# Performance work log

Measured on AMD Instinct MI355X. Metric: run time of the kernel, lower is better.

Reference implementation:

```python
import jax, jax.numpy as jnp
import numpy as np

T, LDIMS, HID, HID2 = 768, 256, 512, 512


def setup_inputs() -> dict:
    key = jax.random.key(0)
    ks = jax.random.split(key, 8)
    s = 0.05  # small init scale keeps tanh out of saturation
    return {
        "x": jax.random.normal(ks[0], (T, 2, LDIMS), dtype=jnp.float32),
        "hidLayerFOH": jax.random.normal(ks[1], (2 * LDIMS, HID), dtype=jnp.float32) * s,
        "hidLayerFOM": jax.random.normal(ks[2], (2 * LDIMS, HID), dtype=jnp.float32) * s,
        "catBias": jax.random.normal(ks[3], (2 * HID,), dtype=jnp.float32) * s,
        "hid2Layer": jax.random.normal(ks[4], (2 * HID, HID2), dtype=jnp.float32) * s,
        "hid2Bias": jax.random.normal(ks[5], (HID2,), dtype=jnp.float32) * s,
        "outLayer": jax.random.normal(ks[6], (HID2, 1), dtype=jnp.float32) * s,
        "outBias": jax.random.normal(ks[7], (1,), dtype=jnp.float32) * s,
    }


def reference(x, hidLayerFOH, hidLayerFOM, catBias, hid2Layer, hid2Bias, outLayer, outBias):
    # x: [T, 2, ldims] -> concat forward/backward LSTM states -> [T, 2*ldims]
    xc = x.reshape(x.shape[0], -1)
    Hf = xc @ hidLayerFOH  # [T, HID] headfov per token
    Mf = xc @ hidLayerFOM  # [T, HID] modfov per token
    # Original: tanh(concat([headfov_i, modfov_j]) + catBias) @ hid2Layer.
    # tanh is elementwise, so split the concat: act halves separately, then
    # split hid2Layer into top/bottom blocks — same math, no [T,T,2H] tensor.
    actH = jnp.tanh(Hf + catBias[:HID])   # [T, HID]
    actM = jnp.tanh(Mf + catBias[HID:])   # [T, HID]
    AH = actH @ hid2Layer[:HID]           # [T, HID2]
    AM = actM @ hid2Layer[HID:]           # [T, HID2]
    # Pairwise second layer: Z[i,j] = tanh(AH[i] + AM[j] + hid2Bias)
    Z = jnp.tanh(AH[:, None, :] + AM[None, :, :] + hid2Bias)  # [T, T, HID2]
    scores = jnp.einsum("ijh,h->ij", Z, outLayer[:, 0]) + outBias[0]  # [T, T]
    return scores
```

## Files before the change

### kernel.cpp

```cpp
#include <hip/hip_runtime.h>

#define TT 768
#define KD 512
#define NC 1024
#define RLN2_2 2.8853900817779268f

typedef short short8 __attribute__((ext_vector_type(8)));
typedef float f32x4  __attribute__((ext_vector_type(4)));
typedef float f32x2  __attribute__((ext_vector_type(2)));

__device__ __forceinline__ float fast_exp2(float x) {
#if __has_builtin(__builtin_amdgcn_exp2f)
    return __builtin_amdgcn_exp2f(x);
#else
    return exp2f(x);
#endif
}
__device__ __forceinline__ float fast_rcp(float x) {
#if __has_builtin(__builtin_amdgcn_rcpf)
    return __builtin_amdgcn_rcpf(x);
#else
    return 1.0f / x;
#endif
}
__device__ __forceinline__ float fast_tanh(float x) {
    float e = fast_exp2(x * RLN2_2);
    return fmaf(-2.0f, fast_rcp(e + 1.0f), 1.0f);
}
__device__ __forceinline__ ushort f2bf(float f) {
    uint u = __float_as_uint(f);
    u += 0x7fff + ((u >> 16) & 1);
    return (ushort)(u >> 16);
}

__global__ __launch_bounds__(256) void k_prep(
    const float* __restrict__ x, const float* __restrict__ foh,
    const float* __restrict__ fom, const float* __restrict__ hid2,
    ushort* __restrict__ xb, ushort* __restrict__ b1t, ushort* __restrict__ h2t)
{
    const int b = blockIdx.x, t = threadIdx.x;
    if (b < 96) {
        int base = b * 4096 + t * 16;
        #pragma unroll
        for (int q = 0; q < 4; ++q) {
            float4 v = *(const float4*)&x[base + q * 4];
            ushort4 o; o.x = f2bf(v.x); o.y = f2bf(v.y); o.z = f2bf(v.z); o.w = f2bf(v.w);
            *(ushort4*)&xb[base + q * 4] = o;
        }
        return;
    }
    __shared__ float tile[64][65];
    const float* src; ushort* dst; int R, C, r0, c0;
    if (b < 160)      { int bb = b - 96;  src = foh;  dst = b1t;             R = 512;  C = 512; r0 = (bb >> 3) * 64; c0 = (bb & 7) * 64; }
    else if (b < 224) { int bb = b - 160; src = fom;  dst = b1t + 512 * 512; R = 512;  C = 512; r0 = (bb >> 3) * 64; c0 = (bb & 7) * 64; }
    else              { int bb = b - 224; src = hid2; dst = h2t;             R = 1024; C = 512; r0 = (bb >> 3) * 64; c0 = (bb & 7) * 64; }
    const int ty = t >> 4, tx = t & 15;
    #pragma unroll
    for (int q = 0; q < 4; ++q) {
        float4 v = *(const float4*)&src[(r0 + ty + q * 16) * C + c0 + tx * 4];
        tile[ty + q * 16][tx * 4 + 0] = v.x;
        tile[ty + q * 16][tx * 4 + 1] = v.y;
        tile[ty + q * 16][tx * 4 + 2] = v.z;
        tile[ty + q * 16][tx * 4 + 3] = v.w;
    }
    __syncthreads();
    #pragma unroll
    for (int q = 0; q < 4; ++q) {
        int cl = ty + q * 16;
        ushort4 o;
        o.x = f2bf(tile[tx * 4 + 0][cl]);
        o.y = f2bf(tile[tx * 4 + 1][cl]);
        o.z = f2bf(tile[tx * 4 + 2][cl]);
        o.w = f2bf(tile[tx * 4 + 3][cl]);
        *(ushort4*)&dst[(c0 + cl) * R + r0 + tx * 4] = o;
    }
}

__global__ __launch_bounds__(64) void k_gemm1(
    const ushort* __restrict__ xb, const ushort* __restrict__ b1t,
    const float* __restrict__ catBias, ushort* __restrict__ act)
{
    const int lane = threadIdx.x;
    const int n0 = blockIdx.x * 32;
    const int m0 = blockIdx.y * 32;
    const int lrow = lane & 15, lk = (lane >> 4) * 8;

    const ushort* pa0 = &xb[(m0 + lrow) * KD + lk];
    const ushort* pa1 = pa0 + 16 * KD;
    const ushort* pb0 = &b1t[(n0 + lrow) * KD + lk];
    const ushort* pb1 = pb0 + 16 * KD;

    f32x4 acc[2][2] = {};
    #pragma unroll 4
    for (int k0 = 0; k0 < KD; k0 += 32) {
        short8 a0 = *(const short8*)(pa0 + k0);
        short8 a1 = *(const short8*)(pa1 + k0);
        short8 b0 = *(const short8*)(pb0 + k0);
        short8 b1 = *(const short8*)(pb1 + k0);
        acc[0][0] = __builtin_amdgcn_mfma_f32_16x16x32_bf16(a0, b0, acc[0][0], 0, 0, 0);
        acc[0][1] = __builtin_amdgcn_mfma_f32_16x16x32_bf16(a0, b1, acc[0][1], 0, 0, 0);
        acc[1][0] = __builtin_amdgcn_mfma_f32_16x16x32_bf16(a1, b0, acc[1][0], 0, 0, 0);
        acc[1][1] = __builtin_amdgcn_mfma_f32_16x16x32_bf16(a1, b1, acc[1][1], 0, 0, 0);
    }
    const int crow = (lane >> 4) * 4, ccol = lane & 15;
    #pragma unroll
    for (int nf = 0; nf < 2; ++nf) {
        int col = n0 + nf * 16 + ccol;
        float cb = catBias[col];
        #pragma unroll
        for (int mf = 0; mf < 2; ++mf) {
            #pragma unroll
            for (int r = 0; r < 4; ++r) {
                int row = m0 + mf * 16 + crow + r;
                act[row * NC + col] = f2bf(fast_tanh(acc[mf][nf][r] + cb));
            }
        }
    }
}

__global__ __launch_bounds__(64) void k_gemm2(
    const ushort* __restrict__ act, const ushort* __restrict__ h2t,
    const float* __restrict__ hid2Bias, float* __restrict__ pw)
{
    const int lane = threadIdx.x;
    const int n0 = blockIdx.x * 32;
    const int m0 = blockIdx.y * 32;
    const bool top = (blockIdx.x < 16);
    const int koff = top ? 0 : 512;
    const int nc0  = top ? n0 : n0 - 512;
    const int lrow = lane & 15, lk = (lane >> 4) * 8;

    const ushort* pa0 = &act[(m0 + lrow) * NC + koff + lk];
    const ushort* pa1 = pa0 + 16 * NC;
    const ushort* pb0 = &h2t[(nc0 + lrow) * NC + koff + lk];
    const ushort* pb1 = pb0 + 16 * NC;

    f32x4 acc[2][2] = {};
    #pragma unroll 4
    for (int k0 = 0; k0 < KD; k0 += 32) {
        short8 a0 = *(const short8*)(pa0 + k0);
        short8 a1 = *(const short8*)(pa1 + k0);
        short8 b0 = *(const short8*)(pb0 + k0);
        short8 b1 = *(const short8*)(pb1 + k0);
        acc[0][0] = __builtin_amdgcn_mfma_f32_16x16x32_bf16(a0, b0, acc[0][0], 0, 0, 0);
        acc[0][1] = __builtin_amdgcn_mfma_f32_16x16x32_bf16(a0, b1, acc[0][1], 0, 0, 0);
        acc[1][0] = __builtin_amdgcn_mfma_f32_16x16x32_bf16(a1, b0, acc[1][0], 0, 0, 0);
        acc[1][1] = __builtin_amdgcn_mfma_f32_16x16x32_bf16(a1, b1, acc[1][1], 0, 0, 0);
    }
    const int crow = (lane >> 4) * 4, ccol = lane & 15;
    #pragma unroll
    for (int nf = 0; nf < 2; ++nf) {
        int col = n0 + nf * 16 + ccol;
        float hb = top ? hid2Bias[col] : 0.0f;
        #pragma unroll
        for (int mf = 0; mf < 2; ++mf) {
            #pragma unroll
            for (int r = 0; r < 4; ++r) {
                int row = m0 + mf * 16 + crow + r;
                pw[row * NC + col] = fast_exp2(RLN2_2 * (acc[mf][nf][r] + hb));
            }
        }
    }
}

__global__ __launch_bounds__(256) void k_pair(
    const float* __restrict__ pw, const float* __restrict__ w,
    const float* __restrict__ outBias, float* __restrict__ out)
{
    __shared__ float Ea[4][16][18];
    __shared__ float Em[4][16][18];
    __shared__ float wl[512];

    const int t    = threadIdx.x;
    const int wv   = t >> 6, lane = t & 63;
    const int bid  = blockIdx.x;
    const int sw   = (bid & 7) * 288 + (bid >> 3);
    const int it = sw / 48, jt = sw % 48;
    const int i0 = it * 16, j0 = jt * 16;
    const int hb0 = wv * 128;

    *(float2*)&wl[hb0 + lane * 2] = *(const float2*)&w[hb0 + lane * 2];
    {
        float4 wa = *(const float4*)&w[lane * 8];
        float4 wb = *(const float4*)&w[lane * 8 + 4];
        float ls = (wa.x + wa.y) + (wa.z + wa.w) + (wb.x + wb.y) + (wb.z + wb.w);
        #pragma unroll
        for (int d = 1; d < 64; d <<= 1) ls += __shfl_xor(ls, d, 64);
        wl[0] = wl[0];
        __asm__ volatile("" ::: );
        #define LSUM_READY ls
        {
            const float lsum = LSUM_READY;

            const int sr = lane >> 2;
            const int sc = (lane & 3) * 4;
            const float* srcA = &pw[(i0 + sr) * NC + hb0 + sc];
            const float* srcM = &pw[(j0 + sr) * NC + 512 + hb0 + sc];

            const int li = lane >> 3, lj = lane & 7;

            float4 fa = *(const float4*)(srcA);
            float4 fm = *(const float4*)(srcM);

            const f32x2 one2 = {1.0f, 1.0f};
            f32x2 accA[2] = {}, accB[2] = {};

            #pragma unroll 1
            for (int c = 0; c < 8; ++c) {
                const int hh = c * 16;
                *(float4*)&Ea[wv][sr][sc] = fa;
                *(float4*)&Em[wv][sr][sc] = fm;
                if (c < 7) {
                    fa = *(const float4*)(srcA + hh + 16);
                    fm = *(const float4*)(srcM + hh + 16);
                }
                #pragma unroll
                for (int hq = 0; hq < 4; ++hq) {
                    float4 e0 = *(const float4*)&Ea[wv][2 * li    ][hq * 4];
                    float4 e1 = *(const float4*)&Ea[wv][2 * li + 1][hq * 4];
                    float4 f0 = *(const float4*)&Em[wv][2 * lj    ][hq * 4];
                    float4 f1 = *(const float4*)&Em[wv][2 * lj + 1][hq * 4];
                    float4 w4 = *(const float4*)&wl[hb0 + hh + hq * 4];
                    #define PKQUAD(DA, DB, WH, ACCA, ACCB)                   \
                    {                                                        \
                        f32x2 Q  = DA * DB;                                  \
                        float pr = Q.x * Q.y;                                \
                        float R  = fast_rcp(pr);                             \
                        float RW = R * (WH);                                 \
                        f32x2 T  = (f32x2){Q.y, Q.x} * RW;                   \
                        ACCA = __builtin_elementwise_fma(T, DB, ACCA);       \
                        ACCB = __builtin_elementwise_fma(T, DA, ACCB);       \
                    }
                    #define HSTEP(H, S)                                                     \
                    {                                                                       \
                        f32x2 F  = {f0.H, f1.H};                                            \
                        f32x2 D0 = __builtin_elementwise_fma((f32x2){e0.H, e0.H}, F, one2); \
                        f32x2 D1 = __builtin_elementwise_fma((f32x2){e1.H, e1.H}, F, one2); \
                        PKQUAD(D0, D1, w4.H, accA[S], accB[S])                              \
                    }
                    HSTEP(x, 0) HSTEP(y, 1) HSTEP(z, 0) HSTEP(w, 1)
                    #undef HSTEP
                    #undef PKQUAD
                }
            }

            f32x2 s0 = accA[0] + accA[1];
            f32x2 s1 = accB[0] + accB[1];

            float* partial = (float*)Ea;
            __syncthreads();
            if (wv >= 1) {
                float* p = partial + (wv - 1) * 256 + lane * 4;
                p[0] = s0.x; p[1] = s0.y; p[2] = s1.x; p[3] = s1.y;
            }
            __syncthreads();
            if (wv == 0) {
                const float base = lsum + outBias[0];
                float t00 = s0.x, t01 = s0.y, t10 = s1.x, t11 = s1.y;
                #pragma unroll
                for (int q = 0; q < 3; ++q) {
                    const float* p = partial + q * 256 + lane * 4;
                    t00 += p[0]; t01 += p[1]; t10 += p[2]; t11 += p[3];
                }
                const int gi = i0 + 2 * li, gj = j0 + 2 * lj;
                float2 o0, o1;
                o0.x = fmaf(-2.f, t00, base);
                o0.y = fmaf(-2.f, t01, base);
                o1.x = fmaf(-2.f, t10, base);
                o1.y = fmaf(-2.f, t11, base);
                *(float2*)&out[gi * TT + gj]       = o0;
                *(float2*)&out[(gi + 1) * TT + gj] = o1;
            }
        }
        #undef LSUM_READY
    }
}

extern "C" void kernel_launch(void* const* d_in, const int* in_sizes, int n_in,
                              void* d_out, int out_size, void* d_ws, size_t ws_size,
                              hipStream_t stream) {
    const float* x        = (const float*)d_in[0];
    const float* foh      = (const float*)d_in[1];
    const float* fom      = (const float*)d_in[2];
    const float* catBias  = (const float*)d_in[3];
    const float* hid2     = (const float*)d_in[4];
    const float* hid2Bias = (const float*)d_in[5];
    const float* outLayer = (const float*)d_in[6];
    const float* outBias  = (const float*)d_in[7];
    float* out = (float*)d_out;

    char* wsb = (char*)d_ws;
    float*  pw  = (float*)(wsb);
    ushort* act = (ushort*)(wsb + 3145728);
    ushort* xb  = (ushort*)(wsb + 4718592);
    ushort* b1t = (ushort*)(wsb + 5505024);
    ushort* h2t = (ushort*)(wsb + 6553600);

    k_prep <<<dim3(352),    256, 0, stream>>>(x, foh, fom, hid2, xb, b1t, h2t);
    k_gemm1<<<dim3(32, 24),  64, 0, stream>>>(xb, b1t, catBias, act);
    k_gemm2<<<dim3(32, 24),  64, 0, stream>>>(act, h2t, hid2Bias, pw);
    k_pair <<<dim3(2304),   256, 0, stream>>>(pw, outLayer, outBias, out);
}
```

Before: 61.07 us.

## Split-K across two waves in GEMMs and shrink prep blocks to 64 threads

Both GEMM kernels now run two wavefronts per block, each covering half of K. The partial accumulators are reduced through shared memory before the epilogue, which halves the serial K-loop length per wave and doubles the number of waves in flight. The prep kernel switches to 64-thread blocks with 32x32 transpose tiles, so four times as many blocks are launched. The pair kernel is only restructured syntactically by removing a redundant scope and macro. The changes add an LDS reduction and a barrier per GEMM block.

```diff
diff --git a/kernel.cpp b/kernel.cpp
--- a/kernel.cpp
+++ b/kernel.cpp
@@ -33,14 +33,14 @@
     return (ushort)(u >> 16);
 }
 
-__global__ __launch_bounds__(256) void k_prep(
+__global__ __launch_bounds__(64) void k_prep(
     const float* __restrict__ x, const float* __restrict__ foh,
     const float* __restrict__ fom, const float* __restrict__ hid2,
     ushort* __restrict__ xb, ushort* __restrict__ b1t, ushort* __restrict__ h2t)
 {
-    const int b = blockIdx.x, t = threadIdx.x;
-    if (b < 96) {
-        int base = b * 4096 + t * 16;
+    const int b = blockIdx.x, lane = threadIdx.x;
+    if (b < 384) {
+        int base = b * 1024 + lane * 16;
         #pragma unroll
         for (int q = 0; q < 4; ++q) {
             float4 v = *(const float4*)&x[base + q * 4];
@@ -49,24 +49,26 @@
         }
         return;
     }
-    __shared__ float tile[64][65];
-    const float* src; ushort* dst; int R, C, r0, c0;
-    if (b < 160)      { int bb = b - 96;  src = foh;  dst = b1t;             R = 512;  C = 512; r0 = (bb >> 3) * 64; c0 = (bb & 7) * 64; }
-    else if (b < 224) { int bb = b - 160; src = fom;  dst = b1t + 512 * 512; R = 512;  C = 512; r0 = (bb >> 3) * 64; c0 = (bb & 7) * 64; }
-    else              { int bb = b - 224; src = hid2; dst = h2t;             R = 1024; C = 512; r0 = (bb >> 3) * 64; c0 = (bb & 7) * 64; }
-    const int ty = t >> 4, tx = t & 15;
+    __shared__ float tile[32][33];
+    int bb = b - 384;
+    const float* src; ushort* dst; int R, C;
+    if (bb < 256)      { src = foh;  dst = b1t;             R = 512;  C = 512; }
+    else if (bb < 512) { src = fom;  dst = b1t + 512 * 512; R = 512;  C = 512; bb -= 256; }
+    else               { src = hid2; dst = h2t;             R = 1024; C = 512; bb -= 512; }
+    const int r0 = (bb >> 4) * 32, c0 = (bb & 15) * 32;
+    const int ty = lane >> 3, tx = lane & 7;
     #pragma unroll
     for (int q = 0; q < 4; ++q) {
-        float4 v = *(const float4*)&src[(r0 + ty + q * 16) * C + c0 + tx * 4];
-        tile[ty + q * 16][tx * 4 + 0] = v.x;
-        tile[ty + q * 16][tx * 4 + 1] = v.y;
-        tile[ty + q * 16][tx * 4 + 2] = v.z;
-        tile[ty + q * 16][tx * 4 + 3] = v.w;
+        float4 v = *(const float4*)&src[(r0 + ty + q * 8) * C + c0 + tx * 4];
+        tile[ty + q * 8][tx * 4 + 0] = v.x;
+        tile[ty + q * 8][tx * 4 + 1] = v.y;
+        tile[ty + q * 8][tx * 4 + 2] = v.z;
+        tile[ty + q * 8][tx * 4 + 3] = v.w;
     }
     __syncthreads();
     #pragma unroll
     for (int q = 0; q < 4; ++q) {
-        int cl = ty + q * 16;
+        int cl = ty + q * 8;
         ushort4 o;
         o.x = f2bf(tile[tx * 4 + 0][cl]);
         o.y = f2bf(tile[tx * 4 + 1][cl]);
@@ -76,23 +78,26 @@
     }
 }
 
-__global__ __launch_bounds__(64) void k_gemm1(
+__global__ __launch_bounds__(128) void k_gemm1(
     const ushort* __restrict__ xb, const ushort* __restrict__ b1t,
     const float* __restrict__ catBias, ushort* __restrict__ act)
 {
-    const int lane = threadIdx.x;
+    __shared__ float ps[64][20];
+    const int t = threadIdx.x;
+    const int kv = t >> 6, lane = t & 63;
     const int n0 = blockIdx.x * 32;
     const int m0 = blockIdx.y * 32;
     const int lrow = lane & 15, lk = (lane >> 4) * 8;
-
-    const ushort* pa0 = &xb[(m0 + lrow) * KD + lk];
+    const int kbase = kv * 256;
+
+    const ushort* pa0 = &xb[(m0 + lrow) * KD + kbase + lk];
     const ushort* pa1 = pa0 + 16 * KD;
-    const ushort* pb0 = &b1t[(n0 + lrow) * KD + lk];
+    const ushort* pb0 = &b1t[(n0 + lrow) * KD + kbase + lk];
     const ushort* pb1 = pb0 + 16 * KD;
 
     f32x4 acc[2][2] = {};
     #pragma unroll 4
-    for (int k0 = 0; k0 < KD; k0 += 32) {
+    for (int k0 = 0; k0 < 256; k0 += 32) {
         short8 a0 = *(const short8*)(pa0 + k0);
         short8 a1 = *(const short8*)(pa1 + k0);
         short8 b0 = *(const short8*)(pb0 + k0);
@@ -102,42 +107,58 @@
         acc[1][0] = __builtin_amdgcn_mfma_f32_16x16x32_bf16(a1, b0, acc[1][0], 0, 0, 0);
         acc[1][1] = __builtin_amdgcn_mfma_f32_16x16x32_bf16(a1, b1, acc[1][1], 0, 0, 0);
     }
-    const int crow = (lane >> 4) * 4, ccol = lane & 15;
-    #pragma unroll
-    for (int nf = 0; nf < 2; ++nf) {
-        int col = n0 + nf * 16 + ccol;
-        float cb = catBias[col];
-        #pragma unroll
-        for (int mf = 0; mf < 2; ++mf) {
+    if (kv == 1) {
+        *(f32x4*)&ps[lane][0]  = acc[0][0];
+        *(f32x4*)&ps[lane][4]  = acc[0][1];
+        *(f32x4*)&ps[lane][8]  = acc[1][0];
+        *(f32x4*)&ps[lane][12] = acc[1][1];
+    }
+    __syncthreads();
+    if (kv == 0) {
+        acc[0][0] += *(const f32x4*)&ps[lane][0];
+        acc[0][1] += *(const f32x4*)&ps[lane][4];
+        acc[1][0] += *(const f32x4*)&ps[lane][8];
+        acc[1][1] += *(const f32x4*)&ps[lane][12];
+        const int crow = (lane >> 4) * 4, ccol = lane & 15;
+        #pragma unroll
+        for (int nf = 0; nf < 2; ++nf) {
+            int col = n0 + nf * 16 + ccol;
+            float cb = catBias[col];
             #pragma unroll
-            for (int r = 0; r < 4; ++r) {
-                int row = m0 + mf * 16 + crow + r;
-                act[row * NC + col] = f2bf(fast_tanh(acc[mf][nf][r] + cb));
+            for (int mf = 0; mf < 2; ++mf) {
+                #pragma unroll
+                for (int r = 0; r < 4; ++r) {
+                    int row = m0 + mf * 16 + crow + r;
+                    act[row * NC + col] = f2bf(fast_tanh(acc[mf][nf][r] + cb));
+                }
             }
         }
     }
 }
 
-__global__ __launch_bounds__(64) void k_gemm2(
+__global__ __launch_bounds__(128) void k_gemm2(
     const ushort* __restrict__ act, const ushort* __restrict__ h2t,
     const float* __restrict__ hid2Bias, float* __restrict__ pw)
 {
-    const int lane = threadIdx.x;
+    __shared__ float ps[64][20];
+    const int t = threadIdx.x;
+    const int kv = t >> 6, lane = t & 63;
     const int n0 = blockIdx.x * 32;
     const int m0 = blockIdx.y * 32;
     const bool top = (blockIdx.x < 16);
     const int koff = top ? 0 : 512;
     const int nc0  = top ? n0 : n0 - 512;
     const int lrow = lane & 15, lk = (lane >> 4) * 8;
-
-    const ushort* pa0 = &act[(m0 + lrow) * NC + koff + lk];
+    const int kbase = kv * 256;
+
+    const ushort* pa0 = &act[(m0 + lrow) * NC + koff + kbase + lk];
     const ushort* pa1 = pa0 + 16 * NC;
-    const ushort* pb0 = &h2t[(nc0 + lrow) * NC + koff + lk];
+    const ushort* pb0 = &h2t[(nc0 + lrow) * NC + koff + kbase + lk];
     const ushort* pb1 = pb0 + 16 * NC;
 
     f32x4 acc[2][2] = {};
     #pragma unroll 4
-    for (int k0 = 0; k0 < KD; k0 += 32) {
+    for (int k0 = 0; k0 < 256; k0 += 32) {
         short8 a0 = *(const short8*)(pa0 + k0);
         short8 a1 = *(const short8*)(pa1 + k0);
         short8 b0 = *(const short8*)(pb0 + k0);
@@ -147,17 +168,30 @@
         acc[1][0] = __builtin_amdgcn_mfma_f32_16x16x32_bf16(a1, b0, acc[1][0], 0, 0, 0);
         acc[1][1] = __builtin_amdgcn_mfma_f32_16x16x32_bf16(a1, b1, acc[1][1], 0, 0, 0);
     }
-    const int crow = (lane >> 4) * 4, ccol = lane & 15;
-    #pragma unroll
-    for (int nf = 0; nf < 2; ++nf) {
-        int col = n0 + nf * 16 + ccol;
-        float hb = top ? hid2Bias[col] : 0.0f;
-        #pragma unroll
-        for (int mf = 0; mf < 2; ++mf) {
+    if (kv == 1) {
+        *(f32x4*)&ps[lane][0]  = acc[0][0];
+        *(f32x4*)&ps[lane][4]  = acc[0][1];
+        *(f32x4*)&ps[lane][8]  = acc[1][0];
+        *(f32x4*)&ps[lane][12] = acc[1][1];
+    }
+    __syncthreads();
+    if (kv == 0) {
+        acc[0][0] += *(const f32x4*)&ps[lane][0];
+        acc[0][1] += *(const f32x4*)&ps[lane][4];
+        acc[1][0] += *(const f32x4*)&ps[lane][8];
+        acc[1][1] += *(const f32x4*)&ps[lane][12];
+        const int crow = (lane >> 4) * 4, ccol = lane & 15;
+        #pragma unroll
+        for (int nf = 0; nf < 2; ++nf) {
+            int col = n0 + nf * 16 + ccol;
+            float hb = top ? hid2Bias[col] : 0.0f;
             #pragma unroll
-            for (int r = 0; r < 4; ++r) {
-                int row = m0 + mf * 16 + crow + r;
-                pw[row * NC + col] = fast_exp2(RLN2_2 * (acc[mf][nf][r] + hb));
+            for (int mf = 0; mf < 2; ++mf) {
+                #pragma unroll
+                for (int r = 0; r < 4; ++r) {
+                    int row = m0 + mf * 16 + crow + r;
+                    pw[row * NC + col] = fast_exp2(RLN2_2 * (acc[mf][nf][r] + hb));
+                }
             }
         }
     }
@@ -180,99 +214,90 @@
     const int hb0 = wv * 128;
 
     *(float2*)&wl[hb0 + lane * 2] = *(const float2*)&w[hb0 + lane * 2];
-    {
-        float4 wa = *(const float4*)&w[lane * 8];
-        float4 wb = *(const float4*)&w[lane * 8 + 4];
-        float ls = (wa.x + wa.y) + (wa.z + wa.w) + (wb.x + wb.y) + (wb.z + wb.w);
-        #pragma unroll
-        for (int d = 1; d < 64; d <<= 1) ls += __shfl_xor(ls, d, 64);
-        wl[0] = wl[0];
-        __asm__ volatile("" ::: );
-        #define LSUM_READY ls
-        {
-            const float lsum = LSUM_READY;
-
-            const int sr = lane >> 2;
-            const int sc = (lane & 3) * 4;
-            const float* srcA = &pw[(i0 + sr) * NC + hb0 + sc];
-            const float* srcM = &pw[(j0 + sr) * NC + 512 + hb0 + sc];
-
-            const int li = lane >> 3, lj = lane & 7;
-
-            float4 fa = *(const float4*)(srcA);
-            float4 fm = *(const float4*)(srcM);
-
-            const f32x2 one2 = {1.0f, 1.0f};
-            f32x2 accA[2] = {}, accB[2] = {};
-
-            #pragma unroll 1
-            for (int c = 0; c < 8; ++c) {
-                const int hh = c * 16;
-                *(float4*)&Ea[wv][sr][sc] = fa;
-                *(float4*)&Em[wv][sr][sc] = fm;
-                if (c < 7) {
-                    fa = *(const float4*)(srcA + hh + 16);
-                    fm = *(const float4*)(srcM + hh + 16);
-                }
-                #pragma unroll
-                for (int hq = 0; hq < 4; ++hq) {
-                    float4 e0 = *(const float4*)&Ea[wv][2 * li    ][hq * 4];
-                    float4 e1 = *(const float4*)&Ea[wv][2 * li + 1][hq * 4];
-                    float4 f0 = *(const float4*)&Em[wv][2 * lj    ][hq * 4];
-                    float4 f1 = *(const float4*)&Em[wv][2 * lj + 1][hq * 4];
-                    float4 w4 = *(const float4*)&wl[hb0 + hh + hq * 4];
-                    #define PKQUAD(DA, DB, WH, ACCA, ACCB)                   \
-                    {                                                        \
-                        f32x2 Q  = DA * DB;                                  \
-                        float pr = Q.x * Q.y;                                \
-                        float R  = fast_rcp(pr);                             \
-                        float RW = R * (WH);                                 \
-                        f32x2 T  = (f32x2){Q.y, Q.x} * RW;                   \
-                        ACCA = __builtin_elementwise_fma(T, DB, ACCA);       \
-                        ACCB = __builtin_elementwise_fma(T, DA, ACCB);       \
-                    }
-                    #define HSTEP(H, S)                                                     \
-                    {                                                                       \
-                        f32x2 F  = {f0.H, f1.H};                                            \
-                        f32x2 D0 = __builtin_elementwise_fma((f32x2){e0.H, e0.H}, F, one2); \
-                        f32x2 D1 = __builtin_elementwise_fma((f32x2){e1.H, e1.H}, F, one2); \
-                        PKQUAD(D0, D1, w4.H, accA[S], accB[S])                              \
-                    }
-                    HSTEP(x, 0) HSTEP(y, 1) HSTEP(z, 0) HSTEP(w, 1)
-                    #undef HSTEP
-                    #undef PKQUAD
-                }
+    float4 wa = *(const float4*)&w[lane * 8];
+    float4 wb = *(const float4*)&w[lane * 8 + 4];
+    float lsum = (wa.x + wa.y) + (wa.z + wa.w) + (wb.x + wb.y) + (wb.z + wb.w);
+    #pragma unroll
+    for (int d = 1; d < 64; d <<= 1) lsum += __shfl_xor(lsum, d, 64);
+
+    const int sr = lane >> 2;
+    const int sc = (lane & 3) * 4;
+    const float* srcA = &pw[(i0 + sr) * NC + hb0 + sc];
+    const float* srcM = &pw[(j0 + sr) * NC + 512 + hb0 + sc];
+
+    const int li = lane >> 3, lj = lane & 7;
+
+    float4 fa = *(const float4*)(srcA);
+    float4 fm = *(const float4*)(srcM);
+
+    const f32x2 one2 = {1.0f, 1.0f};
+    f32x2 accA[2] = {}, accB[2] = {};
+
+    #pragma unroll 1
+    for (int c = 0; c < 8; ++c) {
+        const int hh = c * 16;
+        *(float4*)&Ea[wv][sr][sc] = fa;
+        *(float4*)&Em[wv][sr][sc] = fm;
+        if (c < 7) {
+            fa = *(const float4*)(srcA + hh + 16);
+            fm = *(const float4*)(srcM + hh + 16);
+        }
+        #pragma unroll
+        for (int hq = 0; hq < 4; ++hq) {
+            float4 e0 = *(const float4*)&Ea[wv][2 * li    ][hq * 4];
+            float4 e1 = *(const float4*)&Ea[wv][2 * li + 1][hq * 4];
+            float4 f0 = *(const float4*)&Em[wv][2 * lj    ][hq * 4];
+            float4 f1 = *(const float4*)&Em[wv][2 * lj + 1][hq * 4];
+            float4 w4 = *(const float4*)&wl[hb0 + hh + hq * 4];
+            #define PKQUAD(DA, DB, WH, ACCA, ACCB)                   \
+            {                                                        \
+                f32x2 Q  = DA * DB;                                  \
+                float pr = Q.x * Q.y;                                \
+                float R  = fast_rcp(pr);                             \
+                float RW = R * (WH);                                 \
+                f32x2 T  = (f32x2){Q.y, Q.x} * RW;                   \
+                ACCA = __builtin_elementwise_fma(T, DB, ACCA);       \
+                ACCB = __builtin_elementwise_fma(T, DA, ACCB);       \
             }
-
-            f32x2 s0 = accA[0] + accA[1];
-            f32x2 s1 = accB[0] + accB[1];
-
-            float* partial = (float*)Ea;
-            __syncthreads();
-            if (wv >= 1) {
-                float* p = partial + (wv - 1) * 256 + lane * 4;
-                p[0] = s0.x; p[1] = s0.y; p[2] = s1.x; p[3] = s1.y;
+            #define HSTEP(H, S)                                                     \
+            {                                                                       \
+                f32x2 F  = {f0.H, f1.H};                                            \
+                f32x2 D0 = __builtin_elementwise_fma((f32x2){e0.H, e0.H}, F, one2); \
+                f32x2 D1 = __builtin_elementwise_fma((f32x2){e1.H, e1.H}, F, one2); \
+                PKQUAD(D0, D1, w4.H, accA[S], accB[S])                              \
             }
-            __syncthreads();
-            if (wv == 0) {
-                const float base = lsum + outBias[0];
-                float t00 = s0.x, t01 = s0.y, t10 = s1.x, t11 = s1.y;
-                #pragma unroll
-                for (int q = 0; q < 3; ++q) {
-                    const float* p = partial + q * 256 + lane * 4;
-                    t00 += p[0]; t01 += p[1]; t10 += p[2]; t11 += p[3];
-                }
-                const int gi = i0 + 2 * li, gj = j0 + 2 * lj;
-                float2 o0, o1;
-                o0.x = fmaf(-2.f, t00, base);
-                o0.y = fmaf(-2.f, t01, base);
-                o1.x = fmaf(-2.f, t10, base);
-                o1.y = fmaf(-2.f, t11, base);
-                *(float2*)&out[gi * TT + gj]       = o0;
-                *(float2*)&out[(gi + 1) * TT + gj] = o1;
-            }
-        }
-        #undef LSUM_READY
+            HSTEP(x, 0) HSTEP(y, 1) HSTEP(z, 0) HSTEP(w, 1)
+            #undef HSTEP
+            #undef PKQUAD
+        }
+    }
+
+    f32x2 s0 = accA[0] + accA[1];
+    f32x2 s1 = accB[0] + accB[1];
+
+    float* partial = (float*)Ea;
+    __syncthreads();
+    if (wv >= 1) {
+        float* p = partial + (wv - 1) * 256 + lane * 4;
+        p[0] = s0.x; p[1] = s0.y; p[2] = s1.x; p[3] = s1.y;
+    }
+    __syncthreads();
+    if (wv == 0) {
+        const float base = lsum + outBias[0];
+        float t00 = s0.x, t01 = s0.y, t10 = s1.x, t11 = s1.y;
+        #pragma unroll
+        for (int q = 0; q < 3; ++q) {
+            const float* p = partial + q * 256 + lane * 4;
+            t00 += p[0]; t01 += p[1]; t10 += p[2]; t11 += p[3];
+        }
+        const int gi = i0 + 2 * li, gj = j0 + 2 * lj;
+        float2 o0, o1;
+        o0.x = fmaf(-2.f, t00, base);
+        o0.y = fmaf(-2.f, t01, base);
+        o1.x = fmaf(-2.f, t10, base);
+        o1.y = fmaf(-2.f, t11, base);
+        *(float2*)&out[gi * TT + gj]       = o0;
+        *(float2*)&out[(gi + 1) * TT + gj] = o1;
     }
 }
 
@@ -296,8 +321,8 @@
     ushort* b1t = (ushort*)(wsb + 5505024);
     ushort* h2t = (ushort*)(wsb + 6553600);
 
-    k_prep <<<dim3(352),    256, 0, stream>>>(x, foh, fom, hid2, xb, b1t, h2t);
-    k_gemm1<<<dim3(32, 24),  64, 0, stream>>>(xb, b1t, catBias, act);
-    k_gemm2<<<dim3(32, 24),  64, 0, stream>>>(act, h2t, hid2Bias, pw);
+    k_prep <<<dim3(1408),    64, 0, stream>>>(x, foh, fom, hid2, xb, b1t, h2t);
+    k_gemm1<<<dim3(32, 24), 128, 0, stream>>>(xb, b1t, catBias, act);
+    k_gemm2<<<dim3(32, 24), 128, 0, stream>>>(act, h2t, hid2Bias, pw);
     k_pair <<<dim3(2304),   256, 0, stream>>>(pw, outLayer, outBias, out);
 }
```

After: 58.84 us. -3.7%, faster.
